# Kernel optimization log

Hardware: AMD Instinct MI355X
Metric: run time of the kernel (lower is better)

Reference implementation:

```python
import jax, jax.numpy as jnp
import numpy as np

N, IN_FEATS, OUT_FEATS = 8192, 512, 256


def setup_inputs() -> dict:
    key = jax.random.key(0)
    k1, k2, k3, k4 = jax.random.split(key, 4)
    feature_mat = jax.random.normal(k1, (N, IN_FEATS), dtype=jnp.float32)
    # Xavier-uniform style init for W and W2
    limW = float(np.sqrt(6.0 / (IN_FEATS + OUT_FEATS)))
    W = jax.random.uniform(k2, (IN_FEATS, OUT_FEATS), minval=-limW, maxval=limW, dtype=jnp.float32)
    limW2 = float(np.sqrt(6.0 / (2 * OUT_FEATS + 1)))
    W2 = jax.random.uniform(k3, (2 * OUT_FEATS, 1), minval=-limW2, maxval=limW2, dtype=jnp.float32)
    adj_mat = jax.random.randint(k4, (N, N), 0, 2, dtype=jnp.int32)
    return {"feature_mat": feature_mat, "W": W, "W2": W2, "adj_mat": adj_mat}


def reference(feature_mat, W, W2, adj_mat):
    out_feats = W.shape[1]
    Wh = feature_mat @ W                      # [N, F']
    Wh1 = Wh @ W2[:out_feats, :]              # [N, 1]
    Wh2 = Wh @ W2[out_feats:, :]              # [N, 1]
    e = Wh1 + Wh2.T                           # [N, N] broadcast add
    e = jnp.where(e > 0, e, 0.2 * e)          # leaky_relu(0.2)
    # NOTE: original masks with ZERO (not -inf) before softmax — faithful.
    e = jnp.where(adj_mat > 0, e, jnp.zeros((), dtype=e.dtype))
    attention = jax.nn.softmax(e, axis=1)     # row softmax over all N
    h_prime = attention @ Wh                  # [N, F']
    return jax.nn.relu(h_prime)
```

## Files before the change

### kernel.cpp

```cpp
#include <hip/hip_runtime.h>
#include <cstdint>
#include <cstddef>

#define NR 8192
#define FOUT 256
#define KIN 512
#define KSPLIT 4
#define JCHUNK (NR / KSPLIT)
#define BKJ 64
#define NSTEP (JCHUNK / BKJ)
#define IROWS 128

typedef __attribute__((ext_vector_type(8))) short bf16x8;
typedef __attribute__((ext_vector_type(4))) float f32x4;

__device__ __forceinline__ unsigned f2bf(float x) {
  unsigned u = __float_as_uint(x);
  u += 0x7fffu + ((u >> 16) & 1u);
  return u >> 16;
}
__device__ __forceinline__ float bf2f(unsigned h) {
  return __uint_as_float(h << 16);
}
__device__ __forceinline__ unsigned fkey(float x) {
  unsigned u = __float_as_uint(x);
  return (u & 0x80000000u) ? ~u : (u | 0x80000000u);
}
__device__ __forceinline__ float fkey_dec(unsigned k) {
  return __uint_as_float((k & 0x80000000u) ? (k ^ 0x80000000u) : ~k);
}

#define GLDS(g, l)                                                            \
  __builtin_amdgcn_global_load_lds(                                           \
      (const __attribute__((address_space(1))) unsigned int*)(g),             \
      (__attribute__((address_space(3))) unsigned int*)(l), 16, 0, 0)

__global__ __launch_bounds__(256) void k0_prep(const float* __restrict__ W,
                                               const float* __restrict__ W2,
                                               float* __restrict__ w1,
                                               float* __restrict__ w2,
                                               char* __restrict__ WTbf,
                                               unsigned* __restrict__ maxkey) {
  if (blockIdx.x == 0 && threadIdx.x == 0) *maxkey = 0u;
  int wv = threadIdx.x >> 6, lane = threadIdx.x & 63;
  int k = blockIdx.x * 4 + wv;
  int f4 = lane * 4;
  float4 wr = *(const float4*)(W + (size_t)k * FOUT + f4);
  float4 a = *(const float4*)(W2 + f4);
  float4 b = *(const float4*)(W2 + FOUT + f4);
  float d1 = wr.x * a.x + wr.y * a.y + wr.z * a.z + wr.w * a.w;
  float d2 = wr.x * b.x + wr.y * b.y + wr.z * b.z + wr.w * b.w;
#pragma unroll
  for (int off = 32; off; off >>= 1) {
    d1 += __shfl_xor(d1, off);
    d2 += __shfl_xor(d2, off);
  }
  if (lane == 0) {
    w1[k] = d1;
    w2[k] = d2;
  }
  int kt = k >> 5, kl = k & 31;
  float wv4[4] = {wr.x, wr.y, wr.z, wr.w};
#pragma unroll
  for (int ff = 0; ff < 4; ++ff) {
    int f = f4 + ff;
    size_t addr = (size_t)kt * 16384 + (f >> 4) * 1024 +
                  (((f & 15) | (((kl >> 3) & 3) << 4)) * 16) + (kl & 7) * 2;
    *(unsigned short*)(WTbf + addr) = (unsigned short)f2bf(wv4[ff]);
  }
}

__global__ __launch_bounds__(256) void k2_fused(
    const float* __restrict__ X, const char* __restrict__ WTbf,
    const float* __restrict__ w1, const float* __restrict__ w2,
    char* __restrict__ WhTf, float* __restrict__ Wh1, float* __restrict__ Wh2,
    unsigned* __restrict__ maxkey) {
  __shared__ char smem[2 * 18432 + 4096];
  char* buf0 = smem;
  char* buf1 = smem + 18432;
  char* wlds = smem + 2 * 18432;
  int t = threadIdx.x, wv = t >> 6, lane = t & 63;
  int jb = blockIdx.x * 32;
  int jr = t >> 3, koff = (t & 7) * 4;
  int cA = (jr & 15) | (((koff >> 3) & 3) << 4);
  int swA = cA ^ (((cA >> 4) & 3) << 2);
  int aoff = (jr >> 4) * 1024 + swA * 16 + ((koff & 4) << 1);
  int slotR = lane ^ (((lane >> 4) & 3) << 2);
  const float* xrow = X + (size_t)(jb + jr) * KIN + koff;

  {
    float2 a_ = *(const float2*)(w1 + t * 2);
    float2 b_ = *(const float2*)(w2 + t * 2);
    *(float2*)(wlds + t * 8) = a_;
    *(float2*)(wlds + 2048 + t * 8) = b_;
  }
  __syncthreads();

  float4 st0, st1, st2, st3;
  float d1 = 0.f, d2 = 0.f;
  f32x4 acc[2][4];
#pragma unroll
  for (int a = 0; a < 2; ++a)
#pragma unroll
    for (int b = 0; b < 4; ++b) acc[a][b] = (f32x4){0.f, 0.f, 0.f, 0.f};

#define K2_GLB(KT, BUFW)                                                      \
  do {                                                                        \
    const char* gs_ = WTbf + ((size_t)(KT) << 14) + (wv << 12) + lane * 16;   \
    char* ld_ = (BUFW) + 2048 + (wv << 12);                                   \
    GLDS(gs_, ld_);                                                           \
    GLDS(gs_ + 1024, ld_ + 1024);                                             \
    GLDS(gs_ + 2048, ld_ + 2048);                                             \
    GLDS(gs_ + 3072, ld_ + 3072);                                             \
  } while (0)

#define K2_LDX(KT, ST) (ST) = *(const float4*)(xrow + (KT) * 32)

#define K2_AGEN(ST, BUFW, SNUM)                                               \
  do {                                                                        \
    uint2 a_;                                                                 \
    a_.x = f2bf((ST).x) | (f2bf((ST).y) << 16);                               \
    a_.y = f2bf((ST).z) | (f2bf((ST).w) << 16);                               \
    *(uint2*)((BUFW) + aoff) = a_;                                            \
    float4 wa_ = *(const float4*)(wlds + ((SNUM)*32 + koff) * 4);             \
    float4 wb_ = *(const float4*)(wlds + 2048 + ((SNUM)*32 + koff) * 4);      \
    d1 += (ST).x * wa_.x + (ST).y * wa_.y + (ST).z * wa_.z + (ST).w * wa_.w;  \
    d2 += (ST).x * wb_.x + (ST).y * wb_.y + (ST).z * wb_.z + (ST).w * wb_.w;  \
  } while (0)

#define K2_ITER(S, BUFR, BUFW, STC, STF)                                      \
  do {                                                                        \
    int s_ = (S);                                                             \
    if (s_ + 1 < 16) K2_GLB(s_ + 1, BUFW);                                    \
    K2_LDX((s_ + 3 < 16) ? s_ + 3 : 15, STF);                                 \
    if (s_ + 1 < 16) K2_AGEN(STC, BUFW, s_ + 1);                              \
    bf16x8 a0 = *(const bf16x8*)((BUFR) + slotR * 16);                        \
    bf16x8 a1 = *(const bf16x8*)((BUFR) + 1024 + slotR * 16);                 \
    bf16x8 b0 = *(const bf16x8*)((BUFR) + 2048 + (wv * 4 + 0) * 1024 + lane * 16); \
    bf16x8 b1 = *(const bf16x8*)((BUFR) + 2048 + (wv * 4 + 1) * 1024 + lane * 16); \
    bf16x8 b2 = *(const bf16x8*)((BUFR) + 2048 + (wv * 4 + 2) * 1024 + lane * 16); \
    bf16x8 b3 = *(const bf16x8*)((BUFR) + 2048 + (wv * 4 + 3) * 1024 + lane * 16); \
    acc[0][0] = __builtin_amdgcn_mfma_f32_16x16x32_bf16(a0, b0, acc[0][0], 0, 0, 0); \
    acc[0][1] = __builtin_amdgcn_mfma_f32_16x16x32_bf16(a0, b1, acc[0][1], 0, 0, 0); \
    acc[0][2] = __builtin_amdgcn_mfma_f32_16x16x32_bf16(a0, b2, acc[0][2], 0, 0, 0); \
    acc[0][3] = __builtin_amdgcn_mfma_f32_16x16x32_bf16(a0, b3, acc[0][3], 0, 0, 0); \
    acc[1][0] = __builtin_amdgcn_mfma_f32_16x16x32_bf16(a1, b0, acc[1][0], 0, 0, 0); \
    acc[1][1] = __builtin_amdgcn_mfma_f32_16x16x32_bf16(a1, b1, acc[1][1], 0, 0, 0); \
    acc[1][2] = __builtin_amdgcn_mfma_f32_16x16x32_bf16(a1, b2, acc[1][2], 0, 0, 0); \
    acc[1][3] = __builtin_amdgcn_mfma_f32_16x16x32_bf16(a1, b3, acc[1][3], 0, 0, 0); \
    __builtin_amdgcn_sched_barrier(0);                                        \
    asm volatile("s_waitcnt vmcnt(1)");                                       \
    asm volatile("s_waitcnt lgkmcnt(0)");                                     \
    __builtin_amdgcn_s_barrier();                                             \
    __builtin_amdgcn_sched_barrier(0);                                        \
  } while (0)

  K2_GLB(0, buf0);
  K2_LDX(0, st0);
  K2_LDX(1, st1);
  K2_LDX(2, st2);
  K2_AGEN(st0, buf0, 0);
  __builtin_amdgcn_sched_barrier(0);
  asm volatile("s_waitcnt vmcnt(2)");
  asm volatile("s_waitcnt lgkmcnt(0)");
  __builtin_amdgcn_s_barrier();
  __builtin_amdgcn_sched_barrier(0);

  for (int s4 = 0; s4 < 16; s4 += 4) {
    K2_ITER(s4 + 0, buf0, buf1, st1, st3);
    K2_ITER(s4 + 1, buf1, buf0, st2, st0);
    K2_ITER(s4 + 2, buf0, buf1, st3, st1);
    K2_ITER(s4 + 3, buf1, buf0, st0, st2);
  }
#undef K2_ITER
#undef K2_AGEN
#undef K2_LDX
#undef K2_GLB

  int q = lane >> 4;
#pragma unroll
  for (int mi = 0; mi < 2; ++mi)
#pragma unroll
    for (int nn = 0; nn < 4; ++nn) {
      int u2 = wv * 4 + nn;
      int cell = (lane & 15) | ((((mi * 2) + (q >> 1)) & 3) << 4);
      uint2 v;
      v.x = f2bf(acc[mi][nn].x) | (f2bf(acc[mi][nn].y) << 16);
      v.y = f2bf(acc[mi][nn].z) | (f2bf(acc[mi][nn].w) << 16);
      *(uint2*)(buf0 + 2048 + u2 * 1024 + cell * 16 + ((q & 1) << 3)) = v;
    }
  __syncthreads();
  char* wb = WhTf + (size_t)blockIdx.x * 16384;
#pragma unroll
  for (int q2 = 0; q2 < 4; ++q2) {
    uint4 v = *(const uint4*)(buf0 + 2048 + q2 * 4096 + t * 16);
    *(uint4*)(wb + q2 * 4096 + t * 16) = v;
  }

  d1 += __shfl_xor(d1, 1);
  d1 += __shfl_xor(d1, 2);
  d1 += __shfl_xor(d1, 4);
  d2 += __shfl_xor(d2, 1);
  d2 += __shfl_xor(d2, 2);
  d2 += __shfl_xor(d2, 4);
  if ((t & 7) == 0) {
    Wh1[jb + jr] = d1;
    Wh2[jb + jr] = d2;
  }
  float mx = d2;
#pragma unroll
  for (int off = 32; off >= 8; off >>= 1) mx = fmaxf(mx, __shfl_xor(mx, off));
  __shared__ float red[4];
  if (lane == 0) red[wv] = mx;
  __syncthreads();
  if (t == 0) {
    float bm = fmaxf(fmaxf(red[0], red[1]), fmaxf(red[2], red[3]));
    atomicMax(maxkey, fkey(bm));
  }
}

__device__ __forceinline__ uint2 hv4(int4 aq, float4 wq, float wh1, float m,
                                     float enm, float& z) {
  float s0 = wh1 + wq.x, s1 = wh1 + wq.y, s2 = wh1 + wq.z, s3 = wh1 + wq.w;
  s0 = fmaxf(s0, 0.2f * s0);
  s1 = fmaxf(s1, 0.2f * s1);
  s2 = fmaxf(s2, 0.2f * s2);
  s3 = fmaxf(s3, 0.2f * s3);
  float w0 = aq.x > 0 ? __expf(s0 - m) : enm;
  float w1 = aq.y > 0 ? __expf(s1 - m) : enm;
  float w2 = aq.z > 0 ? __expf(s2 - m) : enm;
  float w3 = aq.w > 0 ? __expf(s3 - m) : enm;
  unsigned h0 = f2bf(w0), h1 = f2bf(w1), h2 = f2bf(w2), h3 = f2bf(w3);
  z += bf2f(h0) + bf2f(h1) + bf2f(h2) + bf2f(h3);
  uint2 r;
  r.x = h0 | (h1 << 16);
  r.y = h2 | (h3 << 16);
  return r;
}
__device__ __forceinline__ uint4 hv8(int4 a0, int4 a1, float4 w0, float4 w1,
                                     float wh1, float m, float enm, float& z) {
  uint2 r0 = hv4(a0, w0, wh1, m, enm, z);
  uint2 r1 = hv4(a1, w1, wh1, m, enm, z);
  return (uint4){r0.x, r0.y, r1.x, r1.y};
}

__global__ __launch_bounds__(1024, 4) void k3_attn(
    const int* __restrict__ adj, const char* __restrict__ WhTf,
    const float* __restrict__ Wh1, const float* __restrict__ Wh2,
    const unsigned* __restrict__ maxptr, float* __restrict__ PVp,
    float* __restrict__ Zp) {
  __shared__ char smem[40960];
  char* abuf0 = smem;
  char* abuf1 = smem + 16384;
  char* wlds = smem + 32768;
  int t = threadIdx.x, wv = t >> 6, lane = t & 63;
  int kc = blockIdx.x & 3;
  int ib = blockIdx.x >> 2;
  int ibase = ib * IROWS;
  int jbch = kc * JCHUNK;
  int r0 = t >> 3;
  int j8 = (t & 7) * 8;
  int iglob = ibase + r0;
  float maxwh2 = fkey_dec(*maxptr);
  float wh1 = Wh1[iglob];
  float m = fmaxf(0.f, wh1 + maxwh2);
  float enm = __expf(-m);
  int unitA = (r0 >> 4) * 2 + (j8 >> 5);
  int cA = (r0 & 15) | (((j8 & 31) >> 3) << 4);
  int swA = cA ^ (((cA >> 4) & 3) << 2);
  int aoff = unitA * 1024 + swA * 16;
  int slotR = lane ^ (((lane >> 4) & 3) << 2);
  const int* adjrow = adj + ((size_t)iglob << 13) + jbch + j8;
  int g = wv >> 1, h = wv & 1;
  const char* bbase = WhTf + ((size_t)(kc * 64) << 14) + (size_t)(2 * g) * 1024 +
                      (size_t)lane * 16;
  const char* wl = wlds + j8 * 4;

  *(float2*)(wlds + t * 8) = *(const float2*)(Wh2 + jbch + t * 2);
  __syncthreads();

  bf16x8 bA00, bA01, bA10, bA11, bB00, bB01, bB10, bB11;
  int4 st0_a, st0_b, st1_a, st1_b;
  f32x4 acc[4][2];
#pragma unroll
  for (int a = 0; a < 4; ++a)
#pragma unroll
    for (int b = 0; b < 2; ++b) acc[a][b] = (f32x4){0.f, 0.f, 0.f, 0.f};
  float zacc = 0.f;

#define K3_LDB(S, B00, B01, B10, B11)                                         \
  do {                                                                        \
    int sc_ = (S) < NSTEP ? (S) : NSTEP - 1;                                  \
    const char* bp_ = bbase + (size_t)(2 * sc_) * 16384;                      \
    B00 = *(const bf16x8*)(bp_);                                 \
    B01 = *(const bf16x8*)(bp_ + 16384);                         \
    B10 = *(const bf16x8*)(bp_ + 1024);                          \
    B11 = *(const bf16x8*)(bp_ + 16384 + 1024);                  \
  } while (0)

#define K3_LDA(S, ST)                                                         \
  do {                                                                        \
    int sc_ = (S) < NSTEP ? (S) : NSTEP - 1;                                  \
    ST##_a = *(const int4*)(adjrow + sc_ * BKJ);                              \
    ST##_b = *(const int4*)(adjrow + sc_ * BKJ + 4);                          \
  } while (0)

#define K3_HV(S, AW, STC)                                                     \
  do {                                                                        \
    float4 wq0_ = *(const float4*)(wl + ((S) + 1) * 256);                     \
    float4 wq1_ = *(const float4*)(wl + ((S) + 1) * 256 + 16);                \
    uint4 a_ = hv8(STC##_a, STC##_b, wq0_, wq1_, wh1, m, enm, zacc);          \
    *(uint4*)((AW) + aoff) = a_;                                              \
  } while (0)

#define K3_MFMA(AR, BC00, BC01, BC10, BC11)                                   \
  do {                                                                        \
    _Pragma("unroll")                                                         \
    for (int rf_ = 0; rf_ < 4; ++rf_) {                                       \
      int ub_ = (h * 4 + rf_) * 2;                                            \
      bf16x8 a0_ = *(const bf16x8*)((AR) + (ub_ + 0) * 1024 + slotR * 16);    \
      bf16x8 a1_ = *(const bf16x8*)((AR) + (ub_ + 1) * 1024 + slotR * 16);    \
      acc[rf_][0] = __builtin_amdgcn_mfma_f32_16x16x32_bf16(a0_, BC00, acc[rf_][0], 0, 0, 0); \
      acc[rf_][1] = __builtin_amdgcn_mfma_f32_16x16x32_bf16(a0_, BC10, acc[rf_][1], 0, 0, 0); \
      acc[rf_][0] = __builtin_amdgcn_mfma_f32_16x16x32_bf16(a1_, BC01, acc[rf_][0], 0, 0, 0); \
      acc[rf_][1] = __builtin_amdgcn_mfma_f32_16x16x32_bf16(a1_, BC11, acc[rf_][1], 0, 0, 0); \
    }                                                                         \
  } while (0)

#define K3_TAIL                                                               \
  do {                                                                        \
    __builtin_amdgcn_sched_barrier(0);                                        \
    asm volatile("s_waitcnt lgkmcnt(0)" ::: "memory");                        \
    __builtin_amdgcn_s_barrier();                                             \
    __builtin_amdgcn_sched_barrier(0);                                        \
  } while (0)

#define K3_ITER_H(S, AR, AW, BC00, BC01, BC10, BC11, BF00, BF01, BF10, BF11,  \
                  STC, DO_HV)                                                 \
  do {                                                                        \
    int s_ = (S);                                                             \
    K3_LDB(s_ + 1, BF00, BF01, BF10, BF11);                                   \
    if (DO_HV) K3_HV(s_, AW, STC);                                            \
    K3_LDA(s_ + 3, STC);                                                      \
    K3_MFMA(AR, BC00, BC01, BC10, BC11);                                      \
    K3_TAIL;                                                                  \
  } while (0)

#define K3_ITER_M(S, AR, AW, BC00, BC01, BC10, BC11, BF00, BF01, BF10, BF11,  \
                  STC, DO_HV)                                                 \
  do {                                                                        \
    int s_ = (S);                                                             \
    K3_LDB(s_ + 1, BF00, BF01, BF10, BF11);                                   \
    K3_MFMA(AR, BC00, BC01, BC10, BC11);                                      \
    if (DO_HV) K3_HV(s_, AW, STC);                                            \
    K3_LDA(s_ + 3, STC);                                                      \
    K3_TAIL;                                                                  \
  } while (0)

  K3_LDB(0, bA00, bA01, bA10, bA11);
  int4 adj0a = *(const int4*)(adjrow);
  int4 adj0b = *(const int4*)(adjrow + 4);
  K3_LDA(1, st1);
  K3_LDA(2, st0);
  {
    float4 wq0 = *(const float4*)(wl);
    float4 wq1 = *(const float4*)(wl + 16);
    uint4 a0 = hv8(adj0a, adj0b, wq0, wq1, wh1, m, enm, zacc);
    *(uint4*)(abuf0 + aoff) = a0;
  }
  K3_TAIL;

  if ((wv & 1) == 0) {
    for (int s2 = 0; s2 < NSTEP - 2; s2 += 2) {
      K3_ITER_H(s2 + 0, abuf0, abuf1, bA00, bA01, bA10, bA11, bB00, bB01,
                bB10, bB11, st1, 1);
      K3_ITER_H(s2 + 1, abuf1, abuf0, bB00, bB01, bB10, bB11, bA00, bA01,
                bA10, bA11, st0, 1);
    }
    K3_ITER_H(NSTEP - 2, abuf0, abuf1, bA00, bA01, bA10, bA11, bB00, bB01,
              bB10, bB11, st1, 1);
    K3_ITER_H(NSTEP - 1, abuf1, abuf0, bB00, bB01, bB10, bB11, bA00, bA01,
              bA10, bA11, st0, 0);
  } else {
    for (int s2 = 0; s2 < NSTEP - 2; s2 += 2) {
      K3_ITER_M(s2 + 0, abuf0, abuf1, bA00, bA01, bA10, bA11, bB00, bB01,
                bB10, bB11, st1, 1);
      K3_ITER_M(s2 + 1, abuf1, abuf0, bB00, bB01, bB10, bB11, bA00, bA01,
                bA10, bA11, st0, 1);
    }
    K3_ITER_M(NSTEP - 2, abuf0, abuf1, bA00, bA01, bA10, bA11, bB00, bB01,
              bB10, bB11, st1, 1);
    K3_ITER_M(NSTEP - 1, abuf1, abuf0, bB00, bB01, bB10, bB11, bA00, bA01,
              bA10, bA11, st0, 0);
  }
#undef K3_ITER_H
#undef K3_ITER_M
#undef K3_TAIL
#undef K3_MFMA
#undef K3_HV
#undef K3_LDA
#undef K3_LDB

  zacc += __shfl_xor(zacc, 1);
  zacc += __shfl_xor(zacc, 2);
  zacc += __shfl_xor(zacc, 4);
  if ((t & 7) == 0) Zp[(size_t)kc * NR + iglob] = zacc;
#pragma unroll
  for (int rf = 0; rf < 4; ++rf)
#pragma unroll
    for (int un = 0; un < 2; ++un) {
      int f = (2 * g + un) * 16 + (lane & 15);
      int row0 = ibase + (h * 4 + rf) * 16 + ((lane >> 4) << 2);
      size_t base = ((size_t)kc * NR + row0) * FOUT + f;
      PVp[base + 0 * FOUT] = acc[rf][un].x;
      PVp[base + 1 * FOUT] = acc[rf][un].y;
      PVp[base + 2 * FOUT] = acc[rf][un].z;
      PVp[base + 3 * FOUT] = acc[rf][un].w;
    }
}

__global__ __launch_bounds__(256) void k4_reduce(const float* __restrict__ PVp,
                                                 const float* __restrict__ Zp,
                                                 float* __restrict__ out) {
  int tid = blockIdx.x * 256 + threadIdx.x;
  int i = tid >> 6;
  int f4 = (tid & 63) * 4;
  float z = Zp[i] + Zp[NR + i] + Zp[2 * NR + i] + Zp[3 * NR + i];
  float4 a = {0.f, 0.f, 0.f, 0.f};
#pragma unroll
  for (int c = 0; c < KSPLIT; ++c) {
    float4 p = *(const float4*)(PVp + ((size_t)c * NR + i) * FOUT + f4);
    a.x += p.x;
    a.y += p.y;
    a.z += p.z;
    a.w += p.w;
  }
  float inv = 1.f / z;
  float4 r;
  r.x = fmaxf(a.x * inv, 0.f);
  r.y = fmaxf(a.y * inv, 0.f);
  r.z = fmaxf(a.z * inv, 0.f);
  r.w = fmaxf(a.w * inv, 0.f);
  *(float4*)(out + (size_t)i * FOUT + f4) = r;
}

extern "C" void kernel_launch(void* const* d_in, const int* in_sizes, int n_in,
                              void* d_out, int out_size, void* d_ws,
                              size_t ws_size, hipStream_t stream) {
  const float* X = (const float*)d_in[0];
  const float* W = (const float*)d_in[1];
  const float* W2 = (const float*)d_in[2];
  const int* adj = (const int*)d_in[3];
  float* out = (float*)d_out;
  char* ws = (char*)d_ws;

  const size_t WHT_OFF = 0;
  const size_t WTBF_OFF = (size_t)4 * 1024 * 1024;
  const size_t W1_OFF = WTBF_OFF + 256 * 1024;
  const size_t W2V_OFF = W1_OFF + 2048;
  const size_t WH1_OFF = W2V_OFF + 2048;
  const size_t WH2_OFF = WH1_OFF + 32768;
  const size_t MXK_OFF = WH2_OFF + 32768;
  const size_t ZP_OFF = MXK_OFF + 256;
  const size_t PV_OFF = ZP_OFF + (size_t)KSPLIT * NR * 4;

  char* WhTf = ws + WHT_OFF;
  char* WTbf = ws + WTBF_OFF;
  float* w1 = (float*)(ws + W1_OFF);
  float* w2 = (float*)(ws + W2V_OFF);
  float* Wh1 = (float*)(ws + WH1_OFF);
  float* Wh2 = (float*)(ws + WH2_OFF);
  unsigned* maxkey = (unsigned*)(ws + MXK_OFF);
  float* Zp = (float*)(ws + ZP_OFF);
  float* PVp = (float*)(ws + PV_OFF);

  k0_prep<<<128, 256, 0, stream>>>(W, W2, w1, w2, WTbf, maxkey);
  k2_fused<<<256, 256, 0, stream>>>(X, WTbf, w1, w2, WhTf, Wh1, Wh2, maxkey);
  k3_attn<<<256, 1024, 0, stream>>>(adj, WhTf, Wh1, Wh2, maxkey, PVp, Zp);
  k4_reduce<<<2048, 256, 0, stream>>>(PVp, Zp, out);
}
```

Before: 109.1 us.

## Retile attention kernel to 64 rows by 128 columns with split-K of two

Changes the attention-times-Wh kernel tile from 128 rows x 64 columns with a four-way column split to 64 rows x 128 columns with a two-way split. B fragments are now loaded inside each step just before the MFMAs instead of being prefetched one step ahead, and the MFMA block is wrapped in s_setprio. The final reduce kernel sums only two partial results. This cuts partial-sum traffic and the reduce work, at the cost of fewer rows per block reusing each B load and the loss of B prefetch latency hiding.

```diff
diff --git a/kernel.cpp b/kernel.cpp
--- a/kernel.cpp
+++ b/kernel.cpp
@@ -5,11 +5,11 @@
 #define NR 8192
 #define FOUT 256
 #define KIN 512
-#define KSPLIT 4
+#define KSPLIT 2
 #define JCHUNK (NR / KSPLIT)
-#define BKJ 64
+#define BKJ 128
 #define NSTEP (JCHUNK / BKJ)
-#define IROWS 128
+#define IROWS 64
 
 typedef __attribute__((ext_vector_type(8))) short bf16x8;
 typedef __attribute__((ext_vector_type(4))) float f32x4;
@@ -249,54 +249,43 @@
     const float* __restrict__ Wh1, const float* __restrict__ Wh2,
     const unsigned* __restrict__ maxptr, float* __restrict__ PVp,
     float* __restrict__ Zp) {
-  __shared__ char smem[40960];
+  __shared__ char smem[49152];
   char* abuf0 = smem;
   char* abuf1 = smem + 16384;
   char* wlds = smem + 32768;
   int t = threadIdx.x, wv = t >> 6, lane = t & 63;
-  int kc = blockIdx.x & 3;
-  int ib = blockIdx.x >> 2;
+  int kc = blockIdx.x & 1;
+  int ib = blockIdx.x >> 1;
   int ibase = ib * IROWS;
   int jbch = kc * JCHUNK;
-  int r0 = t >> 3;
-  int j8 = (t & 7) * 8;
+  int r0 = t >> 4;
+  int j8 = (t & 15) * 8;
   int iglob = ibase + r0;
   float maxwh2 = fkey_dec(*maxptr);
   float wh1 = Wh1[iglob];
   float m = fmaxf(0.f, wh1 + maxwh2);
   float enm = __expf(-m);
-  int unitA = (r0 >> 4) * 2 + (j8 >> 5);
+  int unitA = (r0 >> 4) * 4 + (j8 >> 5);
   int cA = (r0 & 15) | (((j8 & 31) >> 3) << 4);
   int swA = cA ^ (((cA >> 4) & 3) << 2);
   int aoff = unitA * 1024 + swA * 16;
   int slotR = lane ^ (((lane >> 4) & 3) << 2);
   const int* adjrow = adj + ((size_t)iglob << 13) + jbch + j8;
   int g = wv >> 1, h = wv & 1;
-  const char* bbase = WhTf + ((size_t)(kc * 64) << 14) + (size_t)(2 * g) * 1024 +
+  const char* bbase = WhTf + ((size_t)(kc * 128) << 14) + (size_t)(2 * g) * 1024 +
                       (size_t)lane * 16;
   const char* wl = wlds + j8 * 4;
 
-  *(float2*)(wlds + t * 8) = *(const float2*)(Wh2 + jbch + t * 2);
+  *(float4*)(wlds + t * 16) = *(const float4*)(Wh2 + jbch + t * 4);
   __syncthreads();
 
-  bf16x8 bA00, bA01, bA10, bA11, bB00, bB01, bB10, bB11;
   int4 st0_a, st0_b, st1_a, st1_b;
-  f32x4 acc[4][2];
-#pragma unroll
-  for (int a = 0; a < 4; ++a)
+  f32x4 acc[2][2];
+#pragma unroll
+  for (int a = 0; a < 2; ++a)
 #pragma unroll
     for (int b = 0; b < 2; ++b) acc[a][b] = (f32x4){0.f, 0.f, 0.f, 0.f};
   float zacc = 0.f;
-
-#define K3_LDB(S, B00, B01, B10, B11)                                         \
-  do {                                                                        \
-    int sc_ = (S) < NSTEP ? (S) : NSTEP - 1;                                  \
-    const char* bp_ = bbase + (size_t)(2 * sc_) * 16384;                      \
-    B00 = *(const bf16x8*)(bp_);                                 \
-    B01 = *(const bf16x8*)(bp_ + 16384);                         \
-    B10 = *(const bf16x8*)(bp_ + 1024);                          \
-    B11 = *(const bf16x8*)(bp_ + 16384 + 1024);                  \
-  } while (0)
 
 #define K3_LDA(S, ST)                                                         \
   do {                                                                        \
@@ -307,24 +296,33 @@
 
 #define K3_HV(S, AW, STC)                                                     \
   do {                                                                        \
-    float4 wq0_ = *(const float4*)(wl + ((S) + 1) * 256);                     \
-    float4 wq1_ = *(const float4*)(wl + ((S) + 1) * 256 + 16);                \
+    float4 wq0_ = *(const float4*)(wl + ((S) + 1) * 512);                     \
+    float4 wq1_ = *(const float4*)(wl + ((S) + 1) * 512 + 16);                \
     uint4 a_ = hv8(STC##_a, STC##_b, wq0_, wq1_, wh1, m, enm, zacc);          \
     *(uint4*)((AW) + aoff) = a_;                                              \
   } while (0)
 
-#define K3_MFMA(AR, BC00, BC01, BC10, BC11)                                   \
-  do {                                                                        \
+#define K3_MFMA(S, AR)                                                        \
+  do {                                                                        \
+    const char* bp_ = bbase + ((size_t)(4 * (S)) << 14);                      \
+    bf16x8 bv[4][2];                                                          \
     _Pragma("unroll")                                                         \
-    for (int rf_ = 0; rf_ < 4; ++rf_) {                                       \
-      int ub_ = (h * 4 + rf_) * 2;                                            \
-      bf16x8 a0_ = *(const bf16x8*)((AR) + (ub_ + 0) * 1024 + slotR * 16);    \
-      bf16x8 a1_ = *(const bf16x8*)((AR) + (ub_ + 1) * 1024 + slotR * 16);    \
-      acc[rf_][0] = __builtin_amdgcn_mfma_f32_16x16x32_bf16(a0_, BC00, acc[rf_][0], 0, 0, 0); \
-      acc[rf_][1] = __builtin_amdgcn_mfma_f32_16x16x32_bf16(a0_, BC10, acc[rf_][1], 0, 0, 0); \
-      acc[rf_][0] = __builtin_amdgcn_mfma_f32_16x16x32_bf16(a1_, BC01, acc[rf_][0], 0, 0, 0); \
-      acc[rf_][1] = __builtin_amdgcn_mfma_f32_16x16x32_bf16(a1_, BC11, acc[rf_][1], 0, 0, 0); \
+    for (int ks_ = 0; ks_ < 4; ++ks_) {                                       \
+      bv[ks_][0] = *(const bf16x8*)(bp_ + ks_ * 16384);                       \
+      bv[ks_][1] = *(const bf16x8*)(bp_ + ks_ * 16384 + 1024);                \
     }                                                                         \
+    __builtin_amdgcn_s_setprio(1);                                            \
+    _Pragma("unroll")                                                         \
+    for (int rf_ = 0; rf_ < 2; ++rf_) {                                       \
+      int rg_ = 2 * h + rf_;                                                  \
+      _Pragma("unroll")                                                       \
+      for (int ks_ = 0; ks_ < 4; ++ks_) {                                     \
+        bf16x8 a_ = *(const bf16x8*)((AR) + (rg_ * 4 + ks_) * 1024 + slotR * 16); \
+        acc[rf_][0] = __builtin_amdgcn_mfma_f32_16x16x32_bf16(a_, bv[ks_][0], acc[rf_][0], 0, 0, 0); \
+        acc[rf_][1] = __builtin_amdgcn_mfma_f32_16x16x32_bf16(a_, bv[ks_][1], acc[rf_][1], 0, 0, 0); \
+      }                                                                       \
+    }                                                                         \
+    __builtin_amdgcn_s_setprio(0);                                            \
   } while (0)
 
 #define K3_TAIL                                                               \
@@ -335,29 +333,22 @@
     __builtin_amdgcn_sched_barrier(0);                                        \
   } while (0)
 
-#define K3_ITER_H(S, AR, AW, BC00, BC01, BC10, BC11, BF00, BF01, BF10, BF11,  \
-                  STC, DO_HV)                                                 \
-  do {                                                                        \
-    int s_ = (S);                                                             \
-    K3_LDB(s_ + 1, BF00, BF01, BF10, BF11);                                   \
-    if (DO_HV) K3_HV(s_, AW, STC);                                            \
-    K3_LDA(s_ + 3, STC);                                                      \
-    K3_MFMA(AR, BC00, BC01, BC10, BC11);                                      \
+#define K3_ITER_H(S, AR, AW, STC, DO_HV)                                      \
+  do {                                                                        \
+    if (DO_HV) K3_HV(S, AW, STC);                                             \
+    K3_LDA((S) + 3, STC);                                                     \
+    K3_MFMA(S, AR);                                                           \
     K3_TAIL;                                                                  \
   } while (0)
 
-#define K3_ITER_M(S, AR, AW, BC00, BC01, BC10, BC11, BF00, BF01, BF10, BF11,  \
-                  STC, DO_HV)                                                 \
-  do {                                                                        \
-    int s_ = (S);                                                             \
-    K3_LDB(s_ + 1, BF00, BF01, BF10, BF11);                                   \
-    K3_MFMA(AR, BC00, BC01, BC10, BC11);                                      \
-    if (DO_HV) K3_HV(s_, AW, STC);                                            \
-    K3_LDA(s_ + 3, STC);                                                      \
+#define K3_ITER_M(S, AR, AW, STC, DO_HV)                                      \
+  do {                                                                        \
+    K3_MFMA(S, AR);                                                           \
+    if (DO_HV) K3_HV(S, AW, STC);                                             \
+    K3_LDA((S) + 3, STC);                                                     \
     K3_TAIL;                                                                  \
   } while (0)
 
-  K3_LDB(0, bA00, bA01, bA10, bA11);
   int4 adj0a = *(const int4*)(adjrow);
   int4 adj0b = *(const int4*)(adjrow + 4);
   K3_LDA(1, st1);
@@ -372,26 +363,18 @@
 
   if ((wv & 1) == 0) {
     for (int s2 = 0; s2 < NSTEP - 2; s2 += 2) {
-      K3_ITER_H(s2 + 0, abuf0, abuf1, bA00, bA01, bA10, bA11, bB00, bB01,
-                bB10, bB11, st1, 1);
-      K3_ITER_H(s2 + 1, abuf1, abuf0, bB00, bB01, bB10, bB11, bA00, bA01,
-                bA10, bA11, st0, 1);
+      K3_ITER_H(s2 + 0, abuf0, abuf1, st1, 1);
+      K3_ITER_H(s2 + 1, abuf1, abuf0, st0, 1);
     }
-    K3_ITER_H(NSTEP - 2, abuf0, abuf1, bA00, bA01, bA10, bA11, bB00, bB01,
-              bB10, bB11, st1, 1);
-    K3_ITER_H(NSTEP - 1, abuf1, abuf0, bB00, bB01, bB10, bB11, bA00, bA01,
-              bA10, bA11, st0, 0);
+    K3_ITER_H(NSTEP - 2, abuf0, abuf1, st1, 1);
+    K3_ITER_H(NSTEP - 1, abuf1, abuf0, st0, 0);
   } else {
     for (int s2 = 0; s2 < NSTEP - 2; s2 += 2) {
-      K3_ITER_M(s2 + 0, abuf0, abuf1, bA00, bA01, bA10, bA11, bB00, bB01,
-                bB10, bB11, st1, 1);
-      K3_ITER_M(s2 + 1, abuf1, abuf0, bB00, bB01, bB10, bB11, bA00, bA01,
-                bA10, bA11, st0, 1);
+      K3_ITER_M(s2 + 0, abuf0, abuf1, st1, 1);
+      K3_ITER_M(s2 + 1, abuf1, abuf0, st0, 1);
     }
-    K3_ITER_M(NSTEP - 2, abuf0, abuf1, bA00, bA01, bA10, bA11, bB00, bB01,
-              bB10, bB11, st1, 1);
-    K3_ITER_M(NSTEP - 1, abuf1, abuf0, bB00, bB01, bB10, bB11, bA00, bA01,
-              bA10, bA11, st0, 0);
+    K3_ITER_M(NSTEP - 2, abuf0, abuf1, st1, 1);
+    K3_ITER_M(NSTEP - 1, abuf1, abuf0, st0, 0);
   }
 #undef K3_ITER_H
 #undef K3_ITER_M
@@ -399,18 +382,18 @@
 #undef K3_MFMA
 #undef K3_HV
 #undef K3_LDA
-#undef K3_LDB
 
   zacc += __shfl_xor(zacc, 1);
   zacc += __shfl_xor(zacc, 2);
   zacc += __shfl_xor(zacc, 4);
-  if ((t & 7) == 0) Zp[(size_t)kc * NR + iglob] = zacc;
-#pragma unroll
-  for (int rf = 0; rf < 4; ++rf)
+  zacc += __shfl_xor(zacc, 8);
+  if ((t & 15) == 0) Zp[(size_t)kc * NR + iglob] = zacc;
+#pragma unroll
+  for (int rf = 0; rf < 2; ++rf)
 #pragma unroll
     for (int un = 0; un < 2; ++un) {
       int f = (2 * g + un) * 16 + (lane & 15);
-      int row0 = ibase + (h * 4 + rf) * 16 + ((lane >> 4) << 2);
+      int row0 = ibase + (2 * h + rf) * 16 + ((lane >> 4) << 2);
       size_t base = ((size_t)kc * NR + row0) * FOUT + f;
       PVp[base + 0 * FOUT] = acc[rf][un].x;
       PVp[base + 1 * FOUT] = acc[rf][un].y;
@@ -425,22 +408,15 @@
   int tid = blockIdx.x * 256 + threadIdx.x;
   int i = tid >> 6;
   int f4 = (tid & 63) * 4;
-  float z = Zp[i] + Zp[NR + i] + Zp[2 * NR + i] + Zp[3 * NR + i];
-  float4 a = {0.f, 0.f, 0.f, 0.f};
-#pragma unroll
-  for (int c = 0; c < KSPLIT; ++c) {
-    float4 p = *(const float4*)(PVp + ((size_t)c * NR + i) * FOUT + f4);
-    a.x += p.x;
-    a.y += p.y;
-    a.z += p.z;
-    a.w += p.w;
-  }
+  float z = Zp[i] + Zp[NR + i];
+  float4 p0 = *(const float4*)(PVp + (size_t)i * FOUT + f4);
+  float4 p1 = *(const float4*)(PVp + ((size_t)NR + i) * FOUT + f4);
   float inv = 1.f / z;
   float4 r;
-  r.x = fmaxf(a.x * inv, 0.f);
-  r.y = fmaxf(a.y * inv, 0.f);
-  r.z = fmaxf(a.z * inv, 0.f);
-  r.w = fmaxf(a.w * inv, 0.f);
+  r.x = fmaxf((p0.x + p1.x) * inv, 0.f);
+  r.y = fmaxf((p0.y + p1.y) * inv, 0.f);
+  r.z = fmaxf((p0.z + p1.z) * inv, 0.f);
+  r.w = fmaxf((p0.w + p1.w) * inv, 0.f);
   *(float4*)(out + (size_t)i * FOUT + f4) = r;
 }
 
```

Result: slower. 121.4 us (+11.3%).
